# Kernel tuning notes

Hardware: AMD Instinct MI355X
Metric: run time of the kernel (lower is better)

The kernel has to match this reference:

```python
import jax, jax.numpy as jnp
import numpy as np

B, S, D, H, F, L = 16, 512, 512, 8, 2048, 3  # L layers: 1 in blocks_1 + 2 in blocks_2
DK = D // H
EPS = 1e-5

def setup_inputs():
    key = jax.random.key(0)
    ks = jax.random.split(key, 10)
    sc = 1.0 / np.sqrt(D)
    return dict(
        q_embed_data=jax.random.normal(ks[0], (B, S, D), jnp.float32),
        qa_embed_data=jax.random.normal(ks[1], (B, S, D), jnp.float32),
        Wk=jax.random.normal(ks[2], (L, D, D), jnp.float32) * sc,
        bk=jnp.zeros((L, D), jnp.float32),
        Wv=jax.random.normal(ks[3], (L, D, D), jnp.float32) * sc,
        bv=jnp.zeros((L, D), jnp.float32),
        Wo=jax.random.normal(ks[4], (L, D, D), jnp.float32) * sc,
        bo=jnp.zeros((L, D), jnp.float32),
        gammas=jax.random.normal(ks[5], (L, H, 1, 1), jnp.float32) * 0.5,
        ln1_g=jnp.ones((L, D), jnp.float32),
        ln1_b=jnp.zeros((L, D), jnp.float32),
        W1=jax.random.normal(ks[6], (L, D, F), jnp.float32) * sc,
        b1=jnp.zeros((L, F), jnp.float32),
        W2=jax.random.normal(ks[7], (L, F, D), jnp.float32) * (1.0 / np.sqrt(F)),
        b2=jnp.zeros((L, D), jnp.float32),
        ln2_g=jnp.ones((L, D), jnp.float32),
        ln2_b=jnp.zeros((L, D), jnp.float32),
    )

def _ln(x, g, b):
    m = jnp.mean(x, -1, keepdims=True)
    v = jnp.mean((x - m) ** 2, -1, keepdims=True)
    return (x - m) * jax.lax.rsqrt(v + EPS) * g + b

def _attention(q, k, v, mask, gamma):
    # q,k,v: [B,H,S,DK]; mask: [1,1,S,S] bool; gamma: [H,1,1]
    scores = jnp.einsum('bhid,bhjd->bhij', q, k) / np.sqrt(DK)
    maskf = mask.astype(scores.dtype)
    # first (no-grad in torch) softmax pass for distance decay
    p = jax.nn.softmax(jnp.where(mask, scores, -1e32), axis=-1) * maskf
    distcum = jnp.cumsum(p, axis=-1)
    disttot = jnp.sum(p, axis=-1, keepdims=True)
    idx = jnp.arange(scores.shape[-1])
    pos = jnp.abs(idx[None, :] - idx[:, None]).astype(scores.dtype)[None, None]
    dist = jax.lax.stop_gradient(
        jnp.sqrt(jnp.clip((disttot - distcum) * pos, 0.0, None)))
    g = -jax.nn.softplus(gamma)[None]  # [1,H,1,1]
    total_effect = jnp.clip(jnp.exp(dist * g), 1e-5, 1e5)
    scores = jnp.where(mask, scores * total_effect, -1e32)
    attn = jax.nn.softmax(scores, axis=-1)
    return jnp.einsum('bhij,bhjd->bhid', attn, v)

def _mha(q_in, k_in, v_in, mask, Wk, bk, Wv, bv, Wo, bo, gamma):
    bsz = q_in.shape[0]
    def proj(x, W, b):
        return (x @ W + b).reshape(bsz, -1, H, DK).transpose(0, 2, 1, 3)
    q = proj(q_in, Wk, bk)  # kq_same=True -> q uses k_linear
    k = proj(k_in, Wk, bk)
    v = proj(v_in, Wv, bv)
    o = _attention(q, k, v, mask, gamma)
    o = o.transpose(0, 2, 1, 3).reshape(bsz, -1, D)
    return o @ Wo + bo

def _block(i, mask, query, key, values, apply_pos, P):
    q2 = _mha(query, key, values, mask, P['Wk'][i], P['bk'][i], P['Wv'][i],
              P['bv'][i], P['Wo'][i], P['bo'][i], P['gammas'][i])
    x = _ln(query + q2, P['ln1_g'][i], P['ln1_b'][i])
    if apply_pos:
        h = jax.nn.relu(x @ P['W1'][i] + P['b1'][i]) @ P['W2'][i] + P['b2'][i]
        x = _ln(x + h, P['ln2_g'][i], P['ln2_b'][i])
    return x

def reference(q_embed_data, qa_embed_data, Wk, bk, Wv, bv, Wo, bo, gammas,
              ln1_g, ln1_b, W1, b1, W2, b2, ln2_g, ln2_b):
    P = dict(Wk=Wk, bk=bk, Wv=Wv, bv=bv, Wo=Wo, bo=bo, gammas=gammas,
             ln1_g=ln1_g, ln1_b=ln1_b, W1=W1, b1=b1, W2=W2, b2=b2,
             ln2_g=ln2_g, ln2_b=ln2_b)
    s = q_embed_data.shape[1]
    mask1 = jnp.tril(jnp.ones((s, s), bool))[None, None]        # mask==1: current+past
    mask0 = jnp.tril(jnp.ones((s, s), bool), -1)[None, None]    # mask==0: strictly past
    y = qa_embed_data
    x = q_embed_data
    y = _block(0, mask1, y, y, y, True, P)    # blocks_1: knowledge encoder
    x = _block(1, mask1, x, x, x, False, P)   # blocks_2: question encoder (no FFN)
    x = _block(2, mask0, x, x, y, True, P)    # blocks_2: knowledge retriever
    return x
```

## Files before the change

### kernel.cpp

```cpp
#include <hip/hip_runtime.h>
#include <hip/hip_bf16.h>

#define Bdim 16
#define Sdim 512
#define Ddim 512
#define Hdim 8
#define DKdim 64
#define Fdim 2048
#define Mrows (Bdim * Sdim)

typedef __attribute__((ext_vector_type(8))) short  frag16;
typedef __attribute__((ext_vector_type(4))) float  f32x4;
typedef __attribute__((ext_vector_type(8))) unsigned short ushort8;
typedef __attribute__((ext_vector_type(4))) unsigned short ushort4v;

#if defined(__has_builtin)
#  if __has_builtin(__builtin_amdgcn_exp2f)
#    define EXP2(x) __builtin_amdgcn_exp2f(x)
#  endif
#endif
#ifndef EXP2
#  define EXP2(x) __expf((x) * 0.6931471805599453f)
#endif
#define SC2 0.18033688011112042f

__device__ __forceinline__ unsigned short f2b(float x) {
    union { float f; unsigned int u; } v; v.f = x;
    unsigned int r = (v.u + 0x7FFFu + ((v.u >> 16) & 1u)) >> 16;
    return (unsigned short)r;
}

__global__ __launch_bounds__(256) void gemm_mfma(
    const __hip_bfloat16* __restrict__ A, const __hip_bfloat16* __restrict__ Bt,
    const float* __restrict__ bias, const float* __restrict__ R,
    float* __restrict__ Cf, unsigned short* __restrict__ Cb,
    int M, int N, int K, int do_relu)
{
    __shared__ short As[2][128 * 32];
    __shared__ short Bs[2][128 * 32];

    const int t = threadIdx.x;
    const int lane = t & 63;
    const int wave = t >> 6;

    const int gx = gridDim.x;
    const int nb = gx * gridDim.y;
    const int lid = blockIdx.x + gx * blockIdx.y;
    const int wid = (lid & 7) * (nb >> 3) + (lid >> 3);
    const int bm = (wid / gx) * 128;
    const int bn = (wid % gx) * 128;

    const int wm = (wave >> 1) * 64;
    const int wn = (wave & 1) * 64;

    f32x4 acc[4][4] = {};
    const int lrow = lane >> 2;
    const int lcol = (lane & 3) * 8;

    auto stage = [&](int k0, int buf) {
#pragma unroll
        for (int i = 0; i < 2; ++i) {
            const int chunk = wave * 2 + i;
            const int row = chunk * 16 + lrow;
            const __hip_bfloat16* ga = A + (size_t)(bm + row) * K + k0 + lcol;
            const __hip_bfloat16* gb = Bt + (size_t)(bn + row) * K + k0 + lcol;
            __builtin_amdgcn_global_load_lds(
                (const __attribute__((address_space(1))) unsigned int*)ga,
                (__attribute__((address_space(3))) unsigned int*)(&As[buf][chunk * 512]),
                16, 0, 0);
            __builtin_amdgcn_global_load_lds(
                (const __attribute__((address_space(1))) unsigned int*)gb,
                (__attribute__((address_space(3))) unsigned int*)(&Bs[buf][chunk * 512]),
                16, 0, 0);
        }
    };

    const int fr = lane & 15;
    const int quad = lane >> 4;
    const int nk = K >> 5;

    stage(0, 0);
    __syncthreads();

    for (int it = 0; it < nk; ++it) {
        const int buf = it & 1;
        if (it + 1 < nk) stage((it + 1) << 5, buf ^ 1);
        frag16 af[4], bfr[4];
#pragma unroll
        for (int i = 0; i < 4; ++i) {
            af[i]  = *(const frag16*)(&As[buf][(wm + i * 16 + fr) * 32 + quad * 8]);
            bfr[i] = *(const frag16*)(&Bs[buf][(wn + i * 16 + fr) * 32 + quad * 8]);
        }
#pragma unroll
        for (int mi = 0; mi < 4; ++mi)
#pragma unroll
            for (int ni = 0; ni < 4; ++ni)
                acc[mi][ni] = __builtin_amdgcn_mfma_f32_16x16x32_bf16(
                    af[mi], bfr[ni], acc[mi][ni], 0, 0, 0);
        __syncthreads();
    }

#pragma unroll
    for (int mi = 0; mi < 4; ++mi) {
#pragma unroll
        for (int r = 0; r < 4; ++r) {
            const int m = bm + wm + mi * 16 + quad * 4 + r;
#pragma unroll
            for (int ni = 0; ni < 4; ++ni) {
                const int n = bn + wn + ni * 16 + fr;
                float v = acc[mi][ni][r] + bias[n];
                if (R) v += R[(size_t)m * N + n];
                if (do_relu) v = fmaxf(v, 0.f);
                if (Cf) Cf[(size_t)m * N + n] = v;
                if (Cb) Cb[(size_t)m * N + n] = f2b(v);
            }
        }
    }
}

__global__ __launch_bounds__(256) void gemm_n64(
    const unsigned short* __restrict__ A0, const unsigned short* __restrict__ A1,
    const unsigned short* __restrict__ B0, const unsigned short* __restrict__ B1,
    const float* __restrict__ bias0, const float* __restrict__ bias1,
    const float* __restrict__ R, float* __restrict__ Cf,
    unsigned short* __restrict__ Cb, unsigned short* __restrict__ CbT,
    int K)
{
    const int NN = 512;
    __shared__ short As[2][128 * 64];
    __shared__ short Bs[2][64 * 64];

    const int trans = blockIdx.z;
    const unsigned short* A  = trans ? A1 : A0;
    const unsigned short* Bt = trans ? B1 : B0;
    const float* bias        = trans ? bias1 : bias0;

    const int t = threadIdx.x;
    const int lane = t & 63;
    const int wave = t >> 6;

    const int lid = blockIdx.x + 8 * blockIdx.y;
    const int wid = (lid & 7) * 64 + (lid >> 3);
    const int bm = (wid >> 3) * 128;
    const int bn = (wid & 7) * 64;

    const int wm = (wave >> 1) * 64;
    const int wn = (wave & 1) * 32;

    f32x4 acc[4][2] = {};

    const int srcslot = (((lane & 7) ^ (lane >> 3)) << 3);
    const int rsub = lane >> 3;

    auto stage = [&](int k0, int buf) {
#pragma unroll
        for (int i = 0; i < 4; ++i) {
            const int row = i * 32 + wave * 8 + rsub;
            const unsigned short* ga = A + (size_t)(bm + row) * K + k0 + srcslot;
            __builtin_amdgcn_global_load_lds(
                (const __attribute__((address_space(1))) unsigned int*)ga,
                (__attribute__((address_space(3))) unsigned int*)(&As[buf][(i * 256 + wave * 64) * 8]),
                16, 0, 0);
        }
#pragma unroll
        for (int i = 0; i < 2; ++i) {
            const int row = i * 32 + wave * 8 + rsub;
            const unsigned short* gb = Bt + (size_t)(bn + row) * K + k0 + srcslot;
            __builtin_amdgcn_global_load_lds(
                (const __attribute__((address_space(1))) unsigned int*)gb,
                (__attribute__((address_space(3))) unsigned int*)(&Bs[buf][(i * 256 + wave * 64) * 8]),
                16, 0, 0);
        }
    };

    const int fr = lane & 15;
    const int quad = lane >> 4;
    const int sw = (fr & 7) << 3;
    const int nk = K >> 6;

    stage(0, 0);
    __syncthreads();

    for (int it = 0; it < nk; ++it) {
        const int buf = it & 1;
        if (it + 1 < nk) stage((it + 1) << 6, buf ^ 1);
        frag16 af[2][4], bfr[2][2];
#pragma unroll
        for (int ks = 0; ks < 2; ++ks) {
            const int col = (ks * 32 + quad * 8) ^ sw;
#pragma unroll
            for (int i = 0; i < 4; ++i)
                af[ks][i] = *(const frag16*)(&As[buf][(wm + i * 16 + fr) * 64 + col]);
#pragma unroll
            for (int i = 0; i < 2; ++i)
                bfr[ks][i] = *(const frag16*)(&Bs[buf][(wn + i * 16 + fr) * 64 + col]);
        }
#pragma unroll
        for (int ks = 0; ks < 2; ++ks)
#pragma unroll
            for (int mi = 0; mi < 4; ++mi)
#pragma unroll
                for (int ni = 0; ni < 2; ++ni)
                    acc[mi][ni] = __builtin_amdgcn_mfma_f32_16x16x32_bf16(
                        af[ks][mi], bfr[ks][ni], acc[mi][ni], 0, 0, 0);
        __syncthreads();
    }

    if (trans) {
#pragma unroll
        for (int mi = 0; mi < 4; ++mi)
#pragma unroll
            for (int ni = 0; ni < 2; ++ni) {
                const int m = bm + wm + mi * 16 + quad * 4;
                const int n = bn + wn + ni * 16 + fr;
                ushort4v o;
#pragma unroll
                for (int r = 0; r < 4; ++r) o[r] = f2b(acc[mi][ni][r] + bias[n]);
                const int bb = m >> 9, s = m & 511;
                const int hh = n >> 6, dd = n & 63;
                *(ushort4v*)(CbT + (((size_t)((bb * Hdim + hh) * DKdim + dd)) << 9) + s) = o;
            }
        return;
    }

#pragma unroll
    for (int mi = 0; mi < 4; ++mi) {
#pragma unroll
        for (int r = 0; r < 4; ++r) {
            const int m = bm + wm + mi * 16 + quad * 4 + r;
#pragma unroll
            for (int ni = 0; ni < 2; ++ni) {
                const int n = bn + wn + ni * 16 + fr;
                float v = acc[mi][ni][r] + bias[n];
                if (R) v += R[(size_t)m * NN + n];
                if (Cf) Cf[(size_t)m * NN + n] = v;
                if (Cb) Cb[(size_t)m * NN + n] = f2b(v);
            }
        }
    }
}

__global__ __launch_bounds__(256) void conv_b(
    const float* __restrict__ X, unsigned short* __restrict__ Y)
{
    const size_t i = ((size_t)blockIdx.x * 256 + threadIdx.x) * 8;
    float4 a = *(const float4*)(X + i);
    float4 b = *(const float4*)(X + i + 4);
    ushort8 o;
    o[0] = f2b(a.x); o[1] = f2b(a.y); o[2] = f2b(a.z); o[3] = f2b(a.w);
    o[4] = f2b(b.x); o[5] = f2b(b.y); o[6] = f2b(b.z); o[7] = f2b(b.w);
    *(ushort8*)(Y + i) = o;
}

__global__ __launch_bounds__(256) void wtrans_all(
    const float* __restrict__ Wk, const float* __restrict__ Wv,
    const float* __restrict__ Wo, const float* __restrict__ W1,
    const float* __restrict__ W2, unsigned short* __restrict__ dst)
{
    const int bid = blockIdx.x;
    const float* src; unsigned short* d; int K, N, tk, tn;
    if (bid < 576) {
        const int mat = bid >> 6, tile = bid & 63;
        const int l = mat / 3, wch = mat % 3;
        const float* W = (wch == 0) ? Wk : (wch == 1) ? Wv : Wo;
        src = W + (size_t)l * 262144;
        d = dst + (size_t)mat * 262144;
        K = 512; N = 512; tn = tile & 7; tk = tile >> 3;
    } else if (bid < 1088) {
        const int idx = bid - 576, l2 = idx >> 8, tile = idx & 255;
        src = W1 + (size_t)(l2 * 2) * (512 * 2048);
        d = dst + 9 * 262144 + (size_t)l2 * (512 * 2048);
        K = 512; N = 2048; tn = tile & 31; tk = tile >> 5;
    } else {
        const int idx = bid - 1088, l2 = idx >> 8, tile = idx & 255;
        src = W2 + (size_t)(l2 * 2) * (2048 * 512);
        d = dst + 9 * 262144 + 2 * (512 * 2048) + (size_t)l2 * (2048 * 512);
        K = 2048; N = 512; tn = tile & 7; tk = tile >> 3;
    }
    const int n0 = tn * 64, k0 = tk * 64;
    __shared__ float T[64][65];
    const int t = threadIdx.x;
    const int kl = t >> 4, n4 = (t & 15) << 2;
#pragma unroll
    for (int it = 0; it < 4; ++it) {
        const int k = kl + it * 16;
        float4 v = *(const float4*)(src + (size_t)(k0 + k) * N + n0 + n4);
        T[n4 + 0][k] = v.x; T[n4 + 1][k] = v.y;
        T[n4 + 2][k] = v.z; T[n4 + 3][k] = v.w;
    }
    __syncthreads();
    const int nl = t >> 3, k8 = (t & 7) << 3;
#pragma unroll
    for (int it = 0; it < 2; ++it) {
        const int n = nl + it * 32;
        ushort8 o;
#pragma unroll
        for (int c = 0; c < 8; ++c) o[c] = f2b(T[n][k8 + c]);
        *(ushort8*)(d + (size_t)(n0 + n) * K + k0 + k8) = o;
    }
}

__global__ __launch_bounds__(256, 8) void attn_flash8(
    const unsigned short* __restrict__ Kb,
    const unsigned short* __restrict__ Vt,
    const float* __restrict__ gam,
    unsigned short* __restrict__ Ob,
    int mask_type)
{
    __shared__ float CTw[16 * 33];
    __shared__ unsigned short Pst[4][16 * 36];
    __shared__ float S1s[4][16];
    __shared__ float S2s[4][16];
    __shared__ float OaccA[16 * 66];
    __shared__ float OaccB[16 * 66];

    const int h = blockIdx.x & 7, b = blockIdx.x >> 3;
    const int rk = blockIdx.y;
    const int tile = mask_type ? (31 - rk) : (rk == 0 ? 0 : 32 - rk);

    const int t = threadIdx.x, lane = t & 63, w = t >> 6;
    const int quad = lane >> 4, fr = lane & 15;
    const int q0 = tile * 16;
    const int iRow = q0 + fr;

    const unsigned short* kbase = Kb + (size_t)b * Sdim * Ddim + h * DKdim;
    const unsigned short* vtb = Vt + (size_t)(b * Hdim + h) * DKdim * Sdim;
    const float gneg2 = -log1pf(__expf(gam[h])) * 1.4426950408889634f;

    frag16 aq0 = *(const frag16*)(kbase + (size_t)(q0 + fr) * Ddim + quad * 8);
    frag16 aq1 = *(const frag16*)(kbase + (size_t)(q0 + fr) * Ddim + 32 + quad * 8);

    float psum = 0.f;
    for (int jn = w; jn <= tile; jn += 4) {
        frag16 k0 = *(const frag16*)(kbase + (size_t)(jn * 16 + fr) * Ddim + quad * 8);
        frag16 k1 = *(const frag16*)(kbase + (size_t)(jn * 16 + fr) * Ddim + 32 + quad * 8);
        f32x4 z = {0.f, 0.f, 0.f, 0.f};
        z = __builtin_amdgcn_mfma_f32_16x16x32_bf16(k0, aq0, z, 0, 0, 0);
        z = __builtin_amdgcn_mfma_f32_16x16x32_bf16(k1, aq1, z, 0, 0, 0);
        float tq = 0.f;
        if (jn < tile) {
#pragma unroll
            for (int r = 0; r < 4; ++r) tq += EXP2(z[r] * SC2);
        } else {
#pragma unroll
            for (int r = 0; r < 4; ++r) {
                const bool valid = mask_type ? (quad * 4 + r <= fr)
                                             : (quad * 4 + r < fr);
                tq += valid ? EXP2(z[r] * SC2) : 0.f;
            }
        }
        psum += tq;
        float tt = tq;
        tt += __shfl_xor(tt, 16);
        tt += __shfl_xor(tt, 32);
        if (quad == 0) CTw[fr * 33 + jn] = tt;
    }
    {
        float s1 = psum;
        s1 += __shfl_xor(s1, 16);
        s1 += __shfl_xor(s1, 32);
        if (lane < 16) S1s[w][lane] = s1;
    }
    __syncthreads();

    if (w == 0 && lane < 16) {
        float run = 0.f;
        for (int jn = tile; jn >= 0; --jn) {
            const float tv = CTw[lane * 33 + jn];
            CTw[lane * 33 + jn] = run;
            run += tv;
        }
    }
    __syncthreads();

    const float rsum1 = 1.f / (S1s[0][fr] + S1s[1][fr] + S1s[2][fr] + S1s[3][fr]);
    unsigned short* Pw = Pst[w];
    const bool fm_blk = (mask_type == 0) && (tile == 0);
    const bool fmrow = fm_blk && (fr == 0);
    const int umax = fm_blk ? (Sdim / 32 - 1) : (tile >> 1);
    float sum2p = 0.f;
    f32x4 oacc[4] = {};

    for (int u = umax - w; u >= 0; u -= 4) {
#pragma unroll
        for (int half = 0; half < 2; ++half) {
            const int jn = 2 * u + half;
            uint2 pku;
            if (jn > tile) {
                const unsigned int pv = fmrow ? 0x3F803F80u : 0u;
                pku.x = pv; pku.y = pv;
                sum2p += fmrow ? 4.f : 0.f;
            } else {
                frag16 k0 = *(const frag16*)(kbase + (size_t)(jn * 16 + fr) * Ddim + quad * 8);
                frag16 k1 = *(const frag16*)(kbase + (size_t)(jn * 16 + fr) * Ddim + 32 + quad * 8);
                f32x4 z = {0.f, 0.f, 0.f, 0.f};
                z = __builtin_amdgcn_mfma_f32_16x16x32_bf16(k0, aq0, z, 0, 0, 0);
                z = __builtin_amdgcn_mfma_f32_16x16x32_bf16(k1, aq1, z, 0, 0, 0);
                const bool full = (jn < tile);
                float s2r[4], lsuf[4];
                float tq = 0.f;
#pragma unroll
                for (int r = 3; r >= 0; --r) {
                    lsuf[r] = tq;
                    s2r[r] = z[r] * SC2;
                    float e1 = EXP2(s2r[r]);
                    if (!full) {
                        const bool valid = mask_type ? (quad * 4 + r <= fr)
                                                     : (quad * 4 + r < fr);
                        e1 = valid ? e1 : 0.f;
                    }
                    tq += e1;
                }
                float incl = tq;
                {
                    float u1 = __shfl_down(incl, 16);
                    incl += (quad < 3) ? u1 : 0.f;
                    float u2 = __shfl_down(incl, 32);
                    incl += (quad < 2) ? u2 : 0.f;
                }
                const float base = CTw[fr * 33 + jn] + (incl - tq);
                const float pos0 = (float)(iRow - (jn * 16 + quad * 4));
                float e2v[4];
#pragma unroll
                for (int r = 0; r < 4; ++r) {
                    const float ratio = (base + lsuf[r]) * rsum1;
                    const float arg = ratio * fabsf(pos0 - (float)r);
                    const float te = fmaxf(EXP2(gneg2 * sqrtf(arg)), 1e-5f);
                    float e2 = EXP2(s2r[r] * te);
                    if (!full) {
                        const bool valid = mask_type ? (quad * 4 + r <= fr)
                                                     : (quad * 4 + r < fr);
                        e2 = valid ? e2 : (fmrow ? 1.f : 0.f);
                    }
                    sum2p += e2;
                    e2v[r] = e2;
                }
                union { __hip_bfloat162 hh; unsigned int u; } c0, c1;
                c0.hh = __float22bfloat162_rn(make_float2(e2v[0], e2v[1]));
                c1.hh = __float22bfloat162_rn(make_float2(e2v[2], e2v[3]));
                pku.x = c0.u; pku.y = c1.u;
            }
            *(uint2*)(Pw + fr * 36 + half * 16 + quad * 4) = pku;
        }
        frag16 pf = *(const frag16*)(Pw + fr * 36 + quad * 8);
        const int jb = u * 32;
#pragma unroll
        for (int dt = 0; dt < 4; ++dt) {
            frag16 vf = *(const frag16*)(vtb + (size_t)(dt * 16 + fr) * Sdim + jb + quad * 8);
            oacc[dt] = __builtin_amdgcn_mfma_f32_16x16x32_bf16(pf, vf, oacc[dt], 0, 0, 0);
        }
    }

    {
        float s2 = sum2p;
        s2 += __shfl_xor(s2, 16);
        s2 += __shfl_xor(s2, 32);
        if (lane < 16) S2s[w][lane] = s2;
    }
    if (w == 1) {
#pragma unroll
        for (int dt = 0; dt < 4; ++dt)
#pragma unroll
            for (int r = 0; r < 4; ++r)
                OaccA[(quad * 4 + r) * 66 + dt * 16 + fr] = oacc[dt][r];
    }
    if (w == 3) {
#pragma unroll
        for (int dt = 0; dt < 4; ++dt)
#pragma unroll
            for (int r = 0; r < 4; ++r)
                OaccB[(quad * 4 + r) * 66 + dt * 16 + fr] = oacc[dt][r];
    }
    __syncthreads();
    if (w == 0) {
#pragma unroll
        for (int dt = 0; dt < 4; ++dt)
#pragma unroll
            for (int r = 0; r < 4; ++r)
                oacc[dt][r] += OaccA[(quad * 4 + r) * 66 + dt * 16 + fr];
    }
    if (w == 2) {
#pragma unroll
        for (int dt = 0; dt < 4; ++dt)
#pragma unroll
            for (int r = 0; r < 4; ++r)
                oacc[dt][r] += OaccB[(quad * 4 + r) * 66 + dt * 16 + fr];
    }
    __syncthreads();
    if (w == 2) {
#pragma unroll
        for (int dt = 0; dt < 4; ++dt)
#pragma unroll
            for (int r = 0; r < 4; ++r)
                OaccA[(quad * 4 + r) * 66 + dt * 16 + fr] = oacc[dt][r];
    }
    __syncthreads();

    if (w == 0) {
        const float rs2 = 1.f / (S2s[0][fr] + S2s[1][fr] + S2s[2][fr] + S2s[3][fr]);
        float rs2q[4];
#pragma unroll
        for (int r = 0; r < 4; ++r) rs2q[r] = __shfl(rs2, quad * 4 + r);

        unsigned short* obase = Ob + ((size_t)(b * Sdim + q0)) * Ddim + h * DKdim;
#pragma unroll
        for (int dt = 0; dt < 4; ++dt)
#pragma unroll
            for (int r = 0; r < 4; ++r) {
                const float v = oacc[dt][r] + OaccA[(quad * 4 + r) * 66 + dt * 16 + fr];
                obase[(size_t)(quad * 4 + r) * Ddim + dt * 16 + fr] = f2b(v * rs2q[r]);
            }
    }
}

__global__ __launch_bounds__(256) void ln_kernel(
    const float* __restrict__ X, const float* __restrict__ g,
    const float* __restrict__ bta, float* __restrict__ Y,
    unsigned short* __restrict__ Yb)
{
    const int row = blockIdx.x;
    const int t = threadIdx.x;
    __shared__ float r1[256], r2[256];
    const float* x = X + (size_t)row * Ddim;
    float a = x[t], b = x[t + 256];
    r1[t] = a + b;
    r2[t] = a * a + b * b;
    __syncthreads();
    for (int off = 128; off; off >>= 1) {
        if (t < off) { r1[t] += r1[t + off]; r2[t] += r2[t + off]; }
        __syncthreads();
    }
    float mean = r1[0] * (1.f / Ddim);
    float var = r2[0] * (1.f / Ddim) - mean * mean;
    float rs = rsqrtf(var + 1e-5f);
    float y0 = (a - mean) * rs * g[t] + bta[t];
    float y1 = (b - mean) * rs * g[t + 256] + bta[t + 256];
    if (Y) {
        float* y = Y + (size_t)row * Ddim;
        y[t] = y0;
        y[t + 256] = y1;
    }
    if (Yb) {
        unsigned short* yb = Yb + (size_t)row * Ddim;
        yb[t] = f2b(y0);
        yb[t + 256] = f2b(y1);
    }
}

extern "C" void kernel_launch(void* const* d_in, const int* in_sizes, int n_in,
                              void* d_out, int out_size, void* d_ws, size_t ws_size,
                              hipStream_t stream)
{
    const float* x0     = (const float*)d_in[0];
    const float* y0     = (const float*)d_in[1];
    const float* Wk     = (const float*)d_in[2];
    const float* bk     = (const float*)d_in[3];
    const float* Wv     = (const float*)d_in[4];
    const float* bv     = (const float*)d_in[5];
    const float* Wo     = (const float*)d_in[6];
    const float* bo     = (const float*)d_in[7];
    const float* gammas = (const float*)d_in[8];
    const float* ln1g   = (const float*)d_in[9];
    const float* ln1b   = (const float*)d_in[10];
    const float* W1     = (const float*)d_in[11];
    const float* b1     = (const float*)d_in[12];
    const float* W2     = (const float*)d_in[13];
    const float* b2     = (const float*)d_in[14];
    const float* ln2g   = (const float*)d_in[15];
    const float* ln2b   = (const float*)d_in[16];

    const size_t NBSD = (size_t)Mrows * Ddim;
    float* ws = (float*)d_ws;
    float* T1   = ws;
    float* X1   = T1 + NBSD;
    float* Xbuf = X1 + NBSD;
    unsigned short* Kbf = (unsigned short*)(Xbuf + NBSD);
    unsigned short* Vt  = Kbf + NBSD;
    unsigned short* AOb = Vt + NBSD;
    unsigned short* Abf = AOb + NBSD;
    unsigned short* Xbf = Abf + NBSD;
    unsigned short* Ybf = Xbf + NBSD;
    unsigned short* Hbb = Ybf + NBSD;
    unsigned short* WtAll = Hbb + (size_t)Mrows * Fdim;

    auto WtK = [&](int l) { return WtAll + (size_t)(l * 3 + 0) * 262144; };
    auto WtV = [&](int l) { return WtAll + (size_t)(l * 3 + 1) * 262144; };
    auto WtO = [&](int l) { return WtAll + (size_t)(l * 3 + 2) * 262144; };
    auto Wt1 = [&](int l) { return WtAll + 9 * 262144 + (size_t)(l >> 1) * (512 * 2048); };
    auto Wt2 = [&](int l) { return WtAll + 9 * 262144 + 2 * (512 * 2048) + (size_t)(l >> 1) * (2048 * 512); };

    const int convBlocks = (int)(NBSD / 2048);

    wtrans_all<<<1600, 256, 0, stream>>>(Wk, Wv, Wo, W1, W2, WtAll);

    auto run_block = [&](int l, const float* qinf, const unsigned short* qinb,
                         const unsigned short* vinb, int mask_type, bool ffn,
                         float* outf, unsigned short* outb) {
        const float* bk_l = bk + (size_t)l * Ddim;
        const float* bv_l = bv + (size_t)l * Ddim;
        const float* bo_l = bo + (size_t)l * Ddim;

        gemm_n64<<<dim3(8, 64, 2), 256, 0, stream>>>(
            qinb, vinb, WtK(l), WtV(l), bk_l, bv_l,
            nullptr, nullptr, Kbf, Vt, Ddim);
        attn_flash8<<<dim3(Bdim * Hdim, Sdim / 16, 1), 256, 0, stream>>>(
            Kbf, Vt, gammas + (size_t)l * Hdim, AOb, mask_type);
        gemm_n64<<<dim3(8, 64, 1), 256, 0, stream>>>(
            AOb, AOb, WtO(l), WtO(l), bo_l, bo_l,
            qinf, T1, nullptr, nullptr, Ddim);
        float* x1f = ffn ? X1 : outf;
        unsigned short* x1b = ffn ? Abf : outb;
        ln_kernel<<<Mrows, 256, 0, stream>>>(T1,
            ln1g + (size_t)l * Ddim, ln1b + (size_t)l * Ddim, x1f, x1b);
        if (ffn) {
            const float* b1_l = b1 + (size_t)l * Fdim;
            const float* b2_l = b2 + (size_t)l * Ddim;
            gemm_mfma<<<dim3(Fdim / 128, Mrows / 128), 256, 0, stream>>>(
                (const __hip_bfloat16*)Abf, (const __hip_bfloat16*)Wt1(l),
                b1_l, nullptr, nullptr, Hbb, Mrows, Fdim, Ddim, 1);
            gemm_n64<<<dim3(8, 64, 1), 256, 0, stream>>>(
                Hbb, Hbb, Wt2(l), Wt2(l), b2_l, b2_l,
                X1, T1, nullptr, nullptr, Fdim);
            ln_kernel<<<Mrows, 256, 0, stream>>>(T1,
                ln2g + (size_t)l * Ddim, ln2b + (size_t)l * Ddim, outf, outb);
        }
    };

    conv_b<<<convBlocks, 256, 0, stream>>>(y0, Abf);
    run_block(0, y0, Abf, Abf, 1, true, nullptr, Ybf);
    conv_b<<<convBlocks, 256, 0, stream>>>(x0, Abf);
    run_block(1, x0, Abf, Abf, 1, false, Xbuf, Xbf);
    run_block(2, Xbuf, Xbf, Ybf, 0, true, (float*)d_out, nullptr);
}
```

Measured before the change: 611.7 us.

## Batch independent layers 0 and 1 into shared dual-layer kernel launches

Layers 0 and 1 read independent inputs, so their bf16 conversion, K/V projections, attention, output projection and first layernorm are now fused into single launches covering both layers (grid z or x doubled). This halves the launch count for that stage and gives each launch twice the blocks, which should fill the GPU better and cut tail effects, especially for the attention kernel. Workspace buffers are reused in new ways (the FFN hidden buffer holds bf16 inputs, and d_out serves as a temporary), and a wrong aliasing choice would corrupt results.

```diff
diff --git a/kernel.cpp b/kernel.cpp
--- a/kernel.cpp
+++ b/kernel.cpp
@@ -240,10 +240,238 @@
     }
 }
 
-__global__ __launch_bounds__(256) void conv_b(
-    const float* __restrict__ X, unsigned short* __restrict__ Y)
-{
-    const size_t i = ((size_t)blockIdx.x * 256 + threadIdx.x) * 8;
+__global__ __launch_bounds__(256) void gemm_kv4(
+    const unsigned short* __restrict__ Ya, const unsigned short* __restrict__ Xa,
+    const unsigned short* __restrict__ BtK0, const unsigned short* __restrict__ BtV0,
+    const unsigned short* __restrict__ BtK1, const unsigned short* __restrict__ BtV1,
+    const float* __restrict__ bk0, const float* __restrict__ bv0,
+    const float* __restrict__ bk1, const float* __restrict__ bv1,
+    unsigned short* __restrict__ K0, unsigned short* __restrict__ V0t,
+    unsigned short* __restrict__ K1, unsigned short* __restrict__ V1t)
+{
+    const int K = 512;
+    __shared__ short As[2][128 * 64];
+    __shared__ short Bs[2][64 * 64];
+
+    const int z = blockIdx.z;
+    const unsigned short* A  = (z < 2) ? Ya : Xa;
+    const unsigned short* Bt = (z == 0) ? BtK0 : (z == 1) ? BtV0 : (z == 2) ? BtK1 : BtV1;
+    const float* bias        = (z == 0) ? bk0 : (z == 1) ? bv0 : (z == 2) ? bk1 : bv1;
+    const int trans = z & 1;
+
+    const int t = threadIdx.x;
+    const int lane = t & 63;
+    const int wave = t >> 6;
+
+    const int lid = blockIdx.x + 8 * blockIdx.y;
+    const int wid = (lid & 7) * 64 + (lid >> 3);
+    const int bm = (wid >> 3) * 128;
+    const int bn = (wid & 7) * 64;
+
+    const int wm = (wave >> 1) * 64;
+    const int wn = (wave & 1) * 32;
+
+    f32x4 acc[4][2] = {};
+    const int srcslot = (((lane & 7) ^ (lane >> 3)) << 3);
+    const int rsub = lane >> 3;
+
+    auto stage = [&](int k0, int buf) {
+#pragma unroll
+        for (int i = 0; i < 4; ++i) {
+            const int row = i * 32 + wave * 8 + rsub;
+            const unsigned short* ga = A + (size_t)(bm + row) * K + k0 + srcslot;
+            __builtin_amdgcn_global_load_lds(
+                (const __attribute__((address_space(1))) unsigned int*)ga,
+                (__attribute__((address_space(3))) unsigned int*)(&As[buf][(i * 256 + wave * 64) * 8]),
+                16, 0, 0);
+        }
+#pragma unroll
+        for (int i = 0; i < 2; ++i) {
+            const int row = i * 32 + wave * 8 + rsub;
+            const unsigned short* gb = Bt + (size_t)(bn + row) * K + k0 + srcslot;
+            __builtin_amdgcn_global_load_lds(
+                (const __attribute__((address_space(1))) unsigned int*)gb,
+                (__attribute__((address_space(3))) unsigned int*)(&Bs[buf][(i * 256 + wave * 64) * 8]),
+                16, 0, 0);
+        }
+    };
+
+    const int fr = lane & 15;
+    const int quad = lane >> 4;
+    const int sw = (fr & 7) << 3;
+    const int nk = K >> 6;
+
+    stage(0, 0);
+    __syncthreads();
+
+    for (int it = 0; it < nk; ++it) {
+        const int buf = it & 1;
+        if (it + 1 < nk) stage((it + 1) << 6, buf ^ 1);
+        frag16 af[2][4], bfr[2][2];
+#pragma unroll
+        for (int ks = 0; ks < 2; ++ks) {
+            const int col = (ks * 32 + quad * 8) ^ sw;
+#pragma unroll
+            for (int i = 0; i < 4; ++i)
+                af[ks][i] = *(const frag16*)(&As[buf][(wm + i * 16 + fr) * 64 + col]);
+#pragma unroll
+            for (int i = 0; i < 2; ++i)
+                bfr[ks][i] = *(const frag16*)(&Bs[buf][(wn + i * 16 + fr) * 64 + col]);
+        }
+#pragma unroll
+        for (int ks = 0; ks < 2; ++ks)
+#pragma unroll
+            for (int mi = 0; mi < 4; ++mi)
+#pragma unroll
+                for (int ni = 0; ni < 2; ++ni)
+                    acc[mi][ni] = __builtin_amdgcn_mfma_f32_16x16x32_bf16(
+                        af[ks][mi], bfr[ks][ni], acc[mi][ni], 0, 0, 0);
+        __syncthreads();
+    }
+
+    if (trans) {
+        unsigned short* CbT = (z == 1) ? V0t : V1t;
+#pragma unroll
+        for (int mi = 0; mi < 4; ++mi)
+#pragma unroll
+            for (int ni = 0; ni < 2; ++ni) {
+                const int m = bm + wm + mi * 16 + quad * 4;
+                const int n = bn + wn + ni * 16 + fr;
+                ushort4v o;
+#pragma unroll
+                for (int r = 0; r < 4; ++r) o[r] = f2b(acc[mi][ni][r] + bias[n]);
+                const int bb = m >> 9, s = m & 511;
+                const int hh = n >> 6, dd = n & 63;
+                *(ushort4v*)(CbT + (((size_t)((bb * Hdim + hh) * DKdim + dd)) << 9) + s) = o;
+            }
+    } else {
+        unsigned short* Cb = (z == 0) ? K0 : K1;
+#pragma unroll
+        for (int mi = 0; mi < 4; ++mi)
+#pragma unroll
+            for (int r = 0; r < 4; ++r) {
+                const int m = bm + wm + mi * 16 + quad * 4 + r;
+#pragma unroll
+                for (int ni = 0; ni < 2; ++ni) {
+                    const int n = bn + wn + ni * 16 + fr;
+                    Cb[(size_t)m * 512 + n] = f2b(acc[mi][ni][r] + bias[n]);
+                }
+            }
+    }
+}
+
+__global__ __launch_bounds__(256) void gemm_o2(
+    const unsigned short* __restrict__ A0, const unsigned short* __restrict__ A1,
+    const unsigned short* __restrict__ B0, const unsigned short* __restrict__ B1,
+    const float* __restrict__ bias0, const float* __restrict__ bias1,
+    const float* __restrict__ R0, const float* __restrict__ R1,
+    float* __restrict__ C0, float* __restrict__ C1)
+{
+    const int K = 512;
+    __shared__ short As[2][128 * 64];
+    __shared__ short Bs[2][64 * 64];
+
+    const int z = blockIdx.z;
+    const unsigned short* A  = z ? A1 : A0;
+    const unsigned short* Bt = z ? B1 : B0;
+    const float* bias        = z ? bias1 : bias0;
+    const float* R           = z ? R1 : R0;
+    float* Cf                = z ? C1 : C0;
+
+    const int t = threadIdx.x;
+    const int lane = t & 63;
+    const int wave = t >> 6;
+
+    const int lid = blockIdx.x + 8 * blockIdx.y;
+    const int wid = (lid & 7) * 64 + (lid >> 3);
+    const int bm = (wid >> 3) * 128;
+    const int bn = (wid & 7) * 64;
+
+    const int wm = (wave >> 1) * 64;
+    const int wn = (wave & 1) * 32;
+
+    f32x4 acc[4][2] = {};
+    const int srcslot = (((lane & 7) ^ (lane >> 3)) << 3);
+    const int rsub = lane >> 3;
+
+    auto stage = [&](int k0, int buf) {
+#pragma unroll
+        for (int i = 0; i < 4; ++i) {
+            const int row = i * 32 + wave * 8 + rsub;
+            const unsigned short* ga = A + (size_t)(bm + row) * K + k0 + srcslot;
+            __builtin_amdgcn_global_load_lds(
+                (const __attribute__((address_space(1))) unsigned int*)ga,
+                (__attribute__((address_space(3))) unsigned int*)(&As[buf][(i * 256 + wave * 64) * 8]),
+                16, 0, 0);
+        }
+#pragma unroll
+        for (int i = 0; i < 2; ++i) {
+            const int row = i * 32 + wave * 8 + rsub;
+            const unsigned short* gb = Bt + (size_t)(bn + row) * K + k0 + srcslot;
+            __builtin_amdgcn_global_load_lds(
+                (const __attribute__((address_space(1))) unsigned int*)gb,
+                (__attribute__((address_space(3))) unsigned int*)(&Bs[buf][(i * 256 + wave * 64) * 8]),
+                16, 0, 0);
+        }
+    };
+
+    const int fr = lane & 15;
+    const int quad = lane >> 4;
+    const int sw = (fr & 7) << 3;
+    const int nk = K >> 6;
+
+    stage(0, 0);
+    __syncthreads();
+
+    for (int it = 0; it < nk; ++it) {
+        const int buf = it & 1;
+        if (it + 1 < nk) stage((it + 1) << 6, buf ^ 1);
+        frag16 af[2][4], bfr[2][2];
+#pragma unroll
+        for (int ks = 0; ks < 2; ++ks) {
+            const int col = (ks * 32 + quad * 8) ^ sw;
+#pragma unroll
+            for (int i = 0; i < 4; ++i)
+                af[ks][i] = *(const frag16*)(&As[buf][(wm + i * 16 + fr) * 64 + col]);
+#pragma unroll
+            for (int i = 0; i < 2; ++i)
+                bfr[ks][i] = *(const frag16*)(&Bs[buf][(wn + i * 16 + fr) * 64 + col]);
+        }
+#pragma unroll
+        for (int ks = 0; ks < 2; ++ks)
+#pragma unroll
+            for (int mi = 0; mi < 4; ++mi)
+#pragma unroll
+                for (int ni = 0; ni < 2; ++ni)
+                    acc[mi][ni] = __builtin_amdgcn_mfma_f32_16x16x32_bf16(
+                        af[ks][mi], bfr[ks][ni], acc[mi][ni], 0, 0, 0);
+        __syncthreads();
+    }
+
+#pragma unroll
+    for (int mi = 0; mi < 4; ++mi) {
+#pragma unroll
+        for (int r = 0; r < 4; ++r) {
+            const int m = bm + wm + mi * 16 + quad * 4 + r;
+#pragma unroll
+            for (int ni = 0; ni < 2; ++ni) {
+                const int n = bn + wn + ni * 16 + fr;
+                Cf[(size_t)m * 512 + n] = acc[mi][ni][r] + bias[n] + R[(size_t)m * 512 + n];
+            }
+        }
+    }
+}
+
+__global__ __launch_bounds__(256) void conv_b2(
+    const float* __restrict__ X0, unsigned short* __restrict__ Y0,
+    const float* __restrict__ X1, unsigned short* __restrict__ Y1,
+    int halfBlocks)
+{
+    const int bid = blockIdx.x;
+    const float* X = (bid < halfBlocks) ? X0 : X1;
+    unsigned short* Y = (bid < halfBlocks) ? Y0 : Y1;
+    const int lb = (bid < halfBlocks) ? bid : bid - halfBlocks;
+    const size_t i = ((size_t)lb * 256 + threadIdx.x) * 8;
     float4 a = *(const float4*)(X + i);
     float4 b = *(const float4*)(X + i + 4);
     ushort8 o;
@@ -301,11 +529,11 @@
 }
 
 __global__ __launch_bounds__(256, 8) void attn_flash8(
-    const unsigned short* __restrict__ Kb,
-    const unsigned short* __restrict__ Vt,
+    const unsigned short* __restrict__ Kb0, const unsigned short* __restrict__ Vt0,
+    const unsigned short* __restrict__ Kb1, const unsigned short* __restrict__ Vt1,
     const float* __restrict__ gam,
-    unsigned short* __restrict__ Ob,
-    int mask_type)
+    unsigned short* __restrict__ Ob0, unsigned short* __restrict__ Ob1,
+    int mask_type, int dual)
 {
     __shared__ float CTw[16 * 33];
     __shared__ unsigned short Pst[4][16 * 36];
@@ -314,7 +542,15 @@
     __shared__ float OaccA[16 * 66];
     __shared__ float OaccB[16 * 66];
 
-    const int h = blockIdx.x & 7, b = blockIdx.x >> 3;
+    int bh, layer;
+    if (dual) { layer = blockIdx.x & 1; bh = blockIdx.x >> 1; }
+    else      { layer = 0;              bh = blockIdx.x; }
+    const unsigned short* Kb = layer ? Kb1 : Kb0;
+    const unsigned short* Vt = layer ? Vt1 : Vt0;
+    unsigned short* Ob       = layer ? Ob1 : Ob0;
+    const float* g           = gam + layer * Hdim;
+
+    const int h = bh & 7, b = bh >> 3;
     const int rk = blockIdx.y;
     const int tile = mask_type ? (31 - rk) : (rk == 0 ? 0 : 32 - rk);
 
@@ -325,7 +561,7 @@
 
     const unsigned short* kbase = Kb + (size_t)b * Sdim * Ddim + h * DKdim;
     const unsigned short* vtb = Vt + (size_t)(b * Hdim + h) * DKdim * Sdim;
-    const float gneg2 = -log1pf(__expf(gam[h])) * 1.4426950408889634f;
+    const float gneg2 = -log1pf(__expf(g[h])) * 1.4426950408889634f;
 
     frag16 aq0 = *(const frag16*)(kbase + (size_t)(q0 + fr) * Ddim + quad * 8);
     frag16 aq1 = *(const frag16*)(kbase + (size_t)(q0 + fr) * Ddim + 32 + quad * 8);
@@ -513,14 +749,12 @@
     }
 }
 
-__global__ __launch_bounds__(256) void ln_kernel(
+__device__ __forceinline__ void ln_row(
     const float* __restrict__ X, const float* __restrict__ g,
     const float* __restrict__ bta, float* __restrict__ Y,
-    unsigned short* __restrict__ Yb)
-{
-    const int row = blockIdx.x;
-    const int t = threadIdx.x;
-    __shared__ float r1[256], r2[256];
+    unsigned short* __restrict__ Yb, int row, int t,
+    float* r1, float* r2)
+{
     const float* x = X + (size_t)row * Ddim;
     float a = x[t], b = x[t + 256];
     r1[t] = a + b;
@@ -545,6 +779,31 @@
         yb[t] = f2b(y0);
         yb[t + 256] = f2b(y1);
     }
+}
+
+__global__ __launch_bounds__(256) void ln_kernel(
+    const float* __restrict__ X, const float* __restrict__ g,
+    const float* __restrict__ bta, float* __restrict__ Y,
+    unsigned short* __restrict__ Yb)
+{
+    __shared__ float r1[256], r2[256];
+    ln_row(X, g, bta, Y, Yb, blockIdx.x, threadIdx.x, r1, r2);
+}
+
+__global__ __launch_bounds__(256) void ln_kernel2(
+    const float* __restrict__ Xa, const float* __restrict__ ga,
+    const float* __restrict__ ba, float* __restrict__ Ya,
+    unsigned short* __restrict__ Yba,
+    const float* __restrict__ Xb, const float* __restrict__ gb,
+    const float* __restrict__ bb, float* __restrict__ Yb2,
+    unsigned short* __restrict__ Ybb)
+{
+    __shared__ float r1[256], r2[256];
+    const int row = blockIdx.x;
+    if (row < Mrows)
+        ln_row(Xa, ga, ba, Ya, Yba, row, threadIdx.x, r1, r2);
+    else
+        ln_row(Xb, gb, bb, Yb2, Ybb, row - Mrows, threadIdx.x, r1, r2);
 }
 
 extern "C" void kernel_launch(void* const* d_in, const int* in_sizes, int n_in,
@@ -583,6 +842,13 @@
     unsigned short* Hbb = Ybf + NBSD;
     unsigned short* WtAll = Hbb + (size_t)Mrows * Fdim;
 
+    unsigned short* Xb_in = Hbb;
+    unsigned short* AOb1  = Hbb + NBSD;
+    unsigned short* Yb_in = Hbb + 2 * NBSD;
+    unsigned short* Kbf1  = Abf;
+    unsigned short* Vt1   = Ybf;
+    float* T1b = (float*)d_out;
+
     auto WtK = [&](int l) { return WtAll + (size_t)(l * 3 + 0) * 262144; };
     auto WtV = [&](int l) { return WtAll + (size_t)(l * 3 + 1) * 262144; };
     auto WtO = [&](int l) { return WtAll + (size_t)(l * 3 + 2) * 262144; };
@@ -592,43 +858,43 @@
     const int convBlocks = (int)(NBSD / 2048);
 
     wtrans_all<<<1600, 256, 0, stream>>>(Wk, Wv, Wo, W1, W2, WtAll);
-
-    auto run_block = [&](int l, const float* qinf, const unsigned short* qinb,
-                         const unsigned short* vinb, int mask_type, bool ffn,
-                         float* outf, unsigned short* outb) {
-        const float* bk_l = bk + (size_t)l * Ddim;
-        const float* bv_l = bv + (size_t)l * Ddim;
-        const float* bo_l = bo + (size_t)l * Ddim;
-
-        gemm_n64<<<dim3(8, 64, 2), 256, 0, stream>>>(
-            qinb, vinb, WtK(l), WtV(l), bk_l, bv_l,
-            nullptr, nullptr, Kbf, Vt, Ddim);
-        attn_flash8<<<dim3(Bdim * Hdim, Sdim / 16, 1), 256, 0, stream>>>(
-            Kbf, Vt, gammas + (size_t)l * Hdim, AOb, mask_type);
-        gemm_n64<<<dim3(8, 64, 1), 256, 0, stream>>>(
-            AOb, AOb, WtO(l), WtO(l), bo_l, bo_l,
-            qinf, T1, nullptr, nullptr, Ddim);
-        float* x1f = ffn ? X1 : outf;
-        unsigned short* x1b = ffn ? Abf : outb;
-        ln_kernel<<<Mrows, 256, 0, stream>>>(T1,
-            ln1g + (size_t)l * Ddim, ln1b + (size_t)l * Ddim, x1f, x1b);
-        if (ffn) {
-            const float* b1_l = b1 + (size_t)l * Fdim;
-            const float* b2_l = b2 + (size_t)l * Ddim;
-            gemm_mfma<<<dim3(Fdim / 128, Mrows / 128), 256, 0, stream>>>(
-                (const __hip_bfloat16*)Abf, (const __hip_bfloat16*)Wt1(l),
-                b1_l, nullptr, nullptr, Hbb, Mrows, Fdim, Ddim, 1);
-            gemm_n64<<<dim3(8, 64, 1), 256, 0, stream>>>(
-                Hbb, Hbb, Wt2(l), Wt2(l), b2_l, b2_l,
-                X1, T1, nullptr, nullptr, Fdim);
-            ln_kernel<<<Mrows, 256, 0, stream>>>(T1,
-                ln2g + (size_t)l * Ddim, ln2b + (size_t)l * Ddim, outf, outb);
-        }
-    };
-
-    conv_b<<<convBlocks, 256, 0, stream>>>(y0, Abf);
-    run_block(0, y0, Abf, Abf, 1, true, nullptr, Ybf);
-    conv_b<<<convBlocks, 256, 0, stream>>>(x0, Abf);
-    run_block(1, x0, Abf, Abf, 1, false, Xbuf, Xbf);
-    run_block(2, Xbuf, Xbf, Ybf, 0, true, (float*)d_out, nullptr);
-}
+    conv_b2<<<2 * convBlocks, 256, 0, stream>>>(y0, Yb_in, x0, Xb_in, convBlocks);
+    gemm_kv4<<<dim3(8, 64, 4), 256, 0, stream>>>(
+        Yb_in, Xb_in, WtK(0), WtV(0), WtK(1), WtV(1),
+        bk, bv, bk + Ddim, bv + Ddim,
+        Kbf, Vt, Kbf1, Vt1);
+    attn_flash8<<<dim3(2 * Bdim * Hdim, Sdim / 16, 1), 256, 0, stream>>>(
+        Kbf, Vt, Kbf1, Vt1, gammas, AOb, AOb1, 1, 1);
+    gemm_o2<<<dim3(8, 64, 2), 256, 0, stream>>>(
+        AOb, AOb1, WtO(0), WtO(1), bo, bo + Ddim, y0, x0, T1, T1b);
+    ln_kernel2<<<2 * Mrows, 256, 0, stream>>>(
+        T1, ln1g, ln1b, X1, Abf,
+        T1b, ln1g + Ddim, ln1b + Ddim, Xbuf, Xbf);
+    gemm_mfma<<<dim3(Fdim / 128, Mrows / 128), 256, 0, stream>>>(
+        (const __hip_bfloat16*)Abf, (const __hip_bfloat16*)Wt1(0),
+        b1, nullptr, nullptr, Hbb, Mrows, Fdim, Ddim, 1);
+    gemm_n64<<<dim3(8, 64, 1), 256, 0, stream>>>(
+        Hbb, Hbb, Wt2(0), Wt2(0), b2, b2,
+        X1, T1, nullptr, nullptr, Fdim);
+    ln_kernel<<<Mrows, 256, 0, stream>>>(T1, ln2g, ln2b, nullptr, Ybf);
+
+    const int l = 2;
+    gemm_n64<<<dim3(8, 64, 2), 256, 0, stream>>>(
+        Xbf, Ybf, WtK(l), WtV(l), bk + l * Ddim, bv + l * Ddim,
+        nullptr, nullptr, Kbf, Vt, Ddim);
+    attn_flash8<<<dim3(Bdim * Hdim, Sdim / 16, 1), 256, 0, stream>>>(
+        Kbf, Vt, Kbf, Vt, gammas + (size_t)l * Hdim, AOb, AOb, 0, 0);
+    gemm_n64<<<dim3(8, 64, 1), 256, 0, stream>>>(
+        AOb, AOb, WtO(l), WtO(l), bo + l * Ddim, bo + l * Ddim,
+        Xbuf, T1, nullptr, nullptr, Ddim);
+    ln_kernel<<<Mrows, 256, 0, stream>>>(T1,
+        ln1g + (size_t)l * Ddim, ln1b + (size_t)l * Ddim, X1, Abf);
+    gemm_mfma<<<dim3(Fdim / 128, Mrows / 128), 256, 0, stream>>>(
+        (const __hip_bfloat16*)Abf, (const __hip_bfloat16*)Wt1(l),
+        b1 + (size_t)l * Fdim, nullptr, nullptr, Hbb, Mrows, Fdim, Ddim, 1);
+    gemm_n64<<<dim3(8, 64, 1), 256, 0, stream>>>(
+        Hbb, Hbb, Wt2(l), Wt2(l), b2 + (size_t)l * Ddim, b2 + (size_t)l * Ddim,
+        X1, T1, nullptr, nullptr, Fdim);
+    ln_kernel<<<Mrows, 256, 0, stream>>>(T1,
+        ln2g + (size_t)l * Ddim, ln2b + (size_t)l * Ddim, (float*)d_out, nullptr);
+}
```

Result: faster. 575.3 us (-5.9%).
